# Kernel optimization log

Measured on AMD Instinct MI355X. Metric: run time of the kernel, lower is better.

## Reference

```python
import jax, jax.numpy as jnp
import numpy as np
from jax import lax

ROUTINGS = 3  # num_routing iterations


def _squash(v):
    # v: [..., num_atoms]
    norm = jnp.linalg.norm(v, axis=-1, keepdims=True)
    norm_sq = norm * norm
    return v / norm * (norm_sq / (1.0 + norm_sq))


def setup_inputs() -> dict:
    key = jax.random.key(0)
    k1, k2 = jax.random.split(key)
    B, H, Wd, Ci, Ai = 16, 32, 32, 8, 32
    k, Co, Ao = 5, 16, 16
    x = jax.random.normal(k1, (B, H, Wd, Ci, Ai), dtype=jnp.float32)
    # he_normal init for conv kernel [k, k, Ai, Co*Ao]
    fan_in = k * k * Ai
    W = jax.random.normal(k2, (k, k, Ai, Co * Ao), dtype=jnp.float32) * np.sqrt(2.0 / fan_in).astype(np.float32)
    b = jnp.full((1, 1, Co, Ao), 0.1, dtype=jnp.float32)  # constant(0.1) init
    return {"x": x, "W": W, "b": b}


def reference(x, W, b):
    B, H, Wd, Ci, Ai = x.shape
    k = W.shape[0]
    Co_Ao = W.shape[3]
    Co, Ao = b.shape[2], b.shape[3]
    # fold input capsules into the batch, conv over atoms
    xr = jnp.transpose(x, (0, 3, 1, 2, 4)).reshape(B * Ci, H, Wd, Ai)
    conv = lax.conv_general_dilated(
        xr, W, window_strides=(1, 1), padding="SAME",
        dimension_numbers=("NHWC", "HWIO", "NHWC"))  # [B*Ci, H, W, Co*Ao]
    Ho, Wo = conv.shape[1], conv.shape[2]
    votes = conv.reshape(B, Ci, Ho, Wo, Co, Ao)
    # biases broadcast over spatial dims: [1,1,Co,Ao] -> [Ho,Wo,Co,Ao]
    biases = jnp.broadcast_to(b, (Ho, Wo, Co, Ao))
    # dynamic routing (softmax variant): logits init to 0
    logits = jnp.zeros((B, Ci, Ho, Wo, Co), dtype=votes.dtype)
    activation = None
    for _ in range(ROUTINGS):
        route = jax.nn.softmax(logits, axis=-1)           # [B,Ci,Ho,Wo,Co]
        preact = jnp.sum(route[..., None] * votes, axis=1) + biases  # [B,Ho,Wo,Co,Ao]
        activation = _squash(preact)
        # agreement: sum over atoms of votes * activation
        logits = logits + jnp.sum(votes * activation[:, None], axis=-1)
    return activation
```

## Files before the change

### kernel.cpp

```cpp
#include <hip/hip_runtime.h>
#include <hip/hip_fp16.h>
#include <math.h>


typedef _Float16 f16;
typedef __attribute__((ext_vector_type(2))) _Float16 f16x2;
typedef __attribute__((ext_vector_type(8))) _Float16 f16x8;
typedef __attribute__((ext_vector_type(4))) float f32x4;

#define STRIDE_CI 1944
#define XB_OFF 0
#define WT_OFF 9437184

#define VIDX(p, cp, ao, co) ((((((p)*4 + (cp))*16 + (ao))*18) + (co)) + ((p) & 1))

static __device__ __forceinline__ float2 up16(unsigned int u) {
    union { unsigned int u; f16 h[2]; } c; c.u = u;
    return make_float2((float)c.h[0], (float)c.h[1]);
}

static __device__ __forceinline__ float fdot2u(unsigned int a, unsigned int b, float c) {
#if __has_builtin(__builtin_amdgcn_fdot2)
    union { unsigned int u; f16x2 h; } ua, ub;
    ua.u = a; ub.u = b;
    return __builtin_amdgcn_fdot2(ua.h, ub.h, c, false);
#else
    const float2 fa = up16(a), fb = up16(b);
    return c + fa.x * fb.x + fa.y * fb.y;
#endif
}

__global__ void prep(const float* __restrict__ x, const float* __restrict__ W,
                     f16* __restrict__ xb, f16* __restrict__ Wt) {
    __shared__ f16 lw[32 * 260];
    const int tid = threadIdx.x;
    const int bid = blockIdx.x;
    if (bid < 4608) {
        const int e4 = (bid * 256 + tid) * 4;
        const int c = e4 & 255;
        const int pix = e4 >> 8;
        const int wp = pix % 36;
        const int t = pix / 36;
        const int h = t & 31;
        const int b = t >> 5;
        const int w = wp - 2;
        f16 o[4] = {(f16)0.f, (f16)0.f, (f16)0.f, (f16)0.f};
        if ((unsigned)w < 32u) {
            const float4 v = *(const float4*)&x[(((b * 32 + h) * 32 + w) * 256) + c];
            o[0] = (f16)v.x; o[1] = (f16)v.y; o[2] = (f16)v.z; o[3] = (f16)v.w;
        }
        *(unsigned long long*)&xb[e4] = *(unsigned long long*)o;
    } else {
        const int k5 = bid - 4608;
        for (int rep = 0; rep < 32; ++rep) {
            const int idx = rep * 256 + tid;
            const int ai = idx >> 8, cc = idx & 255;
            lw[ai * 260 + cc] = (f16)W[(k5 * 32 + ai) * 256 + cc];
        }
        __syncthreads();
        for (int rep = 0; rep < 32; ++rep) {
            const int o = rep * 256 + tid;
            const int cc = o >> 5, ai = o & 31;
            Wt[k5 * 8192 + o] = lw[ai * 260 + cc];
        }
    }
}

__global__ __launch_bounds__(256, 3)
void caps_v7(const f16* __restrict__ xb, const f16* __restrict__ Wt,
             const float* __restrict__ bptr, float* __restrict__ out) {
    __shared__ __align__(16) unsigned char smraw[36864];
    f16* patch = (f16*)smraw;
    unsigned int* vl = (unsigned int*)smraw;
    __shared__ __align__(16) uint4 route_l[8 * 16];
    __shared__ float logit_l[8 * 8 * 17];
    __shared__ float bias_l[256];

    const int tid = threadIdx.x;
    const int lane = tid & 63;
    const int wv = tid >> 6;
    const int bid = blockIdx.x;
    const int w0 = (bid & 3) * 8;
    const int h = (bid >> 2) & 31;
    const int b = bid >> 7;

    bias_l[tid] = bptr[tid];

    for (int e = tid; e < 1920; e += 256) {
        const int pos = e >> 5;
        const int ci = (e >> 2) & 7;
        const int s = e & 3;
        const int dh = pos / 12, dw = pos - dh * 12;
        const int gh = h + dh - 2;
        f16x8 v = {};
        if ((unsigned)gh < 32u)
            v = *(const f16x8*)&xb[(((b * 32 + gh) * 36) + (w0 + dw)) * 256 + ci * 32 + s * 8];
        *(f16x8*)&patch[ci * STRIDE_CI + pos * 32 + s * 8] = v;
    }
    __syncthreads();

    const int g = lane >> 4;
    const int q = lane & 15;
    const f16* aptr = patch + (lane & 7) * STRIDE_CI + ((lane >> 3) & 1) * 32 + g * 8;
    const f16* bbase = Wt + (wv * 64 + q) * 32 + g * 8;

    f32x4 acc[4][4];
#pragma unroll
    for (int rb = 0; rb < 4; ++rb)
#pragma unroll
        for (int ct = 0; ct < 4; ++ct) acc[rb][ct] = (f32x4)0.f;

    f16x8 Bc[4], Bn[4];
    f16x8 Ac[4], An[4];
#pragma unroll
    for (int ct = 0; ct < 4; ++ct) {
        Bc[ct] = *(const f16x8*)(bbase + ct * 512);
        Bn[ct] = *(const f16x8*)(bbase + 8192 + ct * 512);
    }
#pragma unroll
    for (int rb = 0; rb < 4; ++rb)
        Ac[rb] = *(const f16x8*)(aptr + rb * 64);

    int k5 = 0;
#pragma unroll
    for (int kh = 0; kh < 5; ++kh) {
#pragma unroll
        for (int kw = 0; kw < 5; ++kw) {
            if (k5 < 24) {
                const int n = k5 + 1;
                const f16* apn = aptr + ((n / 5) * 12 + (n % 5)) * 32;
#pragma unroll
                for (int rb = 0; rb < 4; ++rb)
                    An[rb] = *(const f16x8*)(apn + rb * 64);
            }
            f16x8 Bf[4];
            if (k5 < 23) {
                const f16* bf = bbase + (k5 + 2) * 8192;
#pragma unroll
                for (int ct = 0; ct < 4; ++ct)
                    Bf[ct] = *(const f16x8*)(bf + ct * 512);
            }
#pragma unroll
            for (int rb = 0; rb < 4; ++rb)
#pragma unroll
                for (int ct = 0; ct < 4; ++ct)
                    acc[rb][ct] = __builtin_amdgcn_mfma_f32_16x16x32_f16(
                        Ac[rb], Bc[ct], acc[rb][ct], 0, 0, 0);
#pragma unroll
            for (int rb = 0; rb < 4; ++rb) Ac[rb] = An[rb];
#pragma unroll
            for (int ct = 0; ct < 4; ++ct) { Bc[ct] = Bn[ct]; Bn[ct] = Bf[ct]; }
            ++k5;
        }
    }
    __syncthreads();

#pragma unroll
    for (int rb = 0; rb < 4; ++rb) {
        const int p = rb * 2 + (g >> 1);
        const int cpb = (g & 1) * 2;
#pragma unroll
        for (int ct = 0; ct < 4; ++ct) {
            const int co = wv * 4 + ct;
            union { f16 h[2]; unsigned int u; } c0, c1;
            c0.h[0] = (f16)acc[rb][ct].x; c0.h[1] = (f16)acc[rb][ct].y;
            c1.h[0] = (f16)acc[rb][ct].z; c1.h[1] = (f16)acc[rb][ct].w;
            vl[VIDX(p, cpb, q, co)] = c0.u;
            vl[VIDX(p, cpb + 1, q, co)] = c1.u;
        }
    }
    __syncthreads();

    const int rp  = tid >> 5;
    const int rco = (tid >> 1) & 15;
    const int aoh = tid & 1;
    unsigned int* route_d = (unsigned int*)route_l;

    for (int it = 0; it < 3; ++it) {
        if (it > 0) {
            for (int i = tid; i < 1024; i += 256) {
                const int pp = i >> 7, ci = (i >> 4) & 7, co = i & 15;
                float lg = logit_l[(pp * 8 + ci) * 17 + co];
                float mx = lg;
#pragma unroll
                for (int m = 1; m < 16; m <<= 1) mx = fmaxf(mx, __shfl_xor(mx, m));
                float e = __expf(lg - mx);
                float s = e;
#pragma unroll
                for (int m = 1; m < 16; m <<= 1) s += __shfl_xor(s, m);
                const float r = e * __builtin_amdgcn_rcpf(s);
                const float rother = __shfl_xor(r, 16);
                if (((tid >> 4) & 1) == 0) {
                    union { f16 h[2]; unsigned int u; } pk;
                    pk.h[0] = (f16)r; pk.h[1] = (f16)rother;
                    route_d[(pp * 16 + co) * 4 + (ci >> 1)] = pk.u;
                }
            }
            __syncthreads();
        }

        uint4 r4;
        if (it == 0) {
            r4.x = r4.y = r4.z = r4.w = 0x2C002C00u;
        } else {
            r4 = route_l[rp * 16 + rco];
        }
        float pr[8];
#pragma unroll
        for (int a8 = 0; a8 < 8; ++a8) {
            const int ao = aoh * 8 + a8;
            float v = bias_l[rco * 16 + ao];
            v = fdot2u(vl[VIDX(rp, 0, ao, rco)], r4.x, v);
            v = fdot2u(vl[VIDX(rp, 1, ao, rco)], r4.y, v);
            v = fdot2u(vl[VIDX(rp, 2, ao, rco)], r4.z, v);
            v = fdot2u(vl[VIDX(rp, 3, ao, rco)], r4.w, v);
            pr[a8] = v;
        }
        float sq = 0.f;
#pragma unroll
        for (int a8 = 0; a8 < 8; ++a8) sq += pr[a8] * pr[a8];
        sq += __shfl_xor(sq, 1);
        const float scale = __builtin_amdgcn_sqrtf(sq) * __builtin_amdgcn_rcpf(1.f + sq);
        float actv[8];
#pragma unroll
        for (int a8 = 0; a8 < 8; ++a8) actv[a8] = pr[a8] * scale;

        if (it < 2) {
            float part[8];
#pragma unroll
            for (int cp = 0; cp < 4; ++cp) {
                float e = 0.f, o = 0.f;
#pragma unroll
                for (int a8 = 0; a8 < 8; ++a8) {
                    const float2 f = up16(vl[VIDX(rp, cp, aoh * 8 + a8, rco)]);
                    e += f.x * actv[a8];
                    o += f.y * actv[a8];
                }
                part[cp * 2] = e; part[cp * 2 + 1] = o;
            }
#pragma unroll
            for (int ci = 0; ci < 8; ++ci) part[ci] += __shfl_xor(part[ci], 1);
            if (aoh == 0) {
#pragma unroll
                for (int ci = 0; ci < 8; ++ci) {
                    float* lp = &logit_l[(rp * 8 + ci) * 17 + rco];
                    if (it == 0) *lp = part[ci];
                    else         *lp += part[ci];
                }
            }
            __syncthreads();
        } else {
            const size_t base = ((size_t)((b * 32 + h) * 32 + w0)) * 256;
            float* dst = out + base + rp * 256 + rco * 16 + aoh * 8;
            *(float4*)dst       = make_float4(actv[0], actv[1], actv[2], actv[3]);
            *(float4*)(dst + 4) = make_float4(actv[4], actv[5], actv[6], actv[7]);
        }
    }
}

extern "C" void kernel_launch(void* const* d_in, const int* in_sizes, int n_in,
                              void* d_out, int out_size, void* d_ws, size_t ws_size,
                              hipStream_t stream) {
    const float* x  = (const float*)d_in[0];
    const float* W  = (const float*)d_in[1];
    const float* bb = (const float*)d_in[2];
    float* out = (float*)d_out;
    f16* xb = (f16*)((char*)d_ws + XB_OFF);
    f16* Wt = (f16*)((char*)d_ws + WT_OFF);

    hipLaunchKernelGGL(prep, dim3(4608 + 25), dim3(256), 0, stream, x, W, xb, Wt);
    hipLaunchKernelGGL(caps_v7, dim3(2048), dim3(256), 0, stream, xb, Wt, bb, out);
}
```

Baseline: 147.4 us.

## Keep routing votes in registers via per-thread contiguous LDS layout

Changes the LDS layout of the votes so each routing thread's 32 packed f16 pairs sit contiguously, then loads them once into registers with vector reads instead of re-reading LDS with scattered scalar accesses every routing iteration. Bias values are also loaded straight from global into registers, dropping the shared bias array. This removes repeated LDS traffic in the routing loop but adds about 32 registers per thread, which may pressure the 3-blocks-per-SM launch bound.

```diff
diff --git a/kernel.cpp b/kernel.cpp
--- a/kernel.cpp
+++ b/kernel.cpp
@@ -11,8 +11,6 @@
 #define STRIDE_CI 1944
 #define XB_OFF 0
 #define WT_OFF 9437184
-
-#define VIDX(p, cp, ao, co) ((((((p)*4 + (cp))*16 + (ao))*18) + (co)) + ((p) & 1))
 
 static __device__ __forceinline__ float2 up16(unsigned int u) {
     union { unsigned int u; f16 h[2]; } c; c.u = u;
@@ -67,14 +65,13 @@
 }
 
 __global__ __launch_bounds__(256, 3)
-void caps_v7(const f16* __restrict__ xb, const f16* __restrict__ Wt,
+void caps_v9(const f16* __restrict__ xb, const f16* __restrict__ Wt,
              const float* __restrict__ bptr, float* __restrict__ out) {
     __shared__ __align__(16) unsigned char smraw[36864];
     f16* patch = (f16*)smraw;
     unsigned int* vl = (unsigned int*)smraw;
     __shared__ __align__(16) uint4 route_l[8 * 16];
     __shared__ float logit_l[8 * 8 * 17];
-    __shared__ float bias_l[256];
 
     const int tid = threadIdx.x;
     const int lane = tid & 63;
@@ -84,7 +81,16 @@
     const int h = (bid >> 2) & 31;
     const int b = bid >> 7;
 
-    bias_l[tid] = bptr[tid];
+    const int rp  = tid >> 5;
+    const int rco = (tid >> 1) & 15;
+    const int aoh = tid & 1;
+    float bia[8];
+    {
+        const float4 b0 = *(const float4*)&bptr[rco * 16 + aoh * 8];
+        const float4 b1 = *(const float4*)&bptr[rco * 16 + aoh * 8 + 4];
+        bia[0] = b0.x; bia[1] = b0.y; bia[2] = b0.z; bia[3] = b0.w;
+        bia[4] = b1.x; bia[5] = b1.y; bia[6] = b1.z; bia[7] = b1.w;
+    }
 
     for (int e = tid; e < 1920; e += 256) {
         const int pos = e >> 5;
@@ -159,22 +165,33 @@
     for (int rb = 0; rb < 4; ++rb) {
         const int p = rb * 2 + (g >> 1);
         const int cpb = (g & 1) * 2;
+        const int rowp = p * 32 + (q >> 3);
 #pragma unroll
         for (int ct = 0; ct < 4; ++ct) {
             const int co = wv * 4 + ct;
             union { f16 h[2]; unsigned int u; } c0, c1;
             c0.h[0] = (f16)acc[rb][ct].x; c0.h[1] = (f16)acc[rb][ct].y;
             c1.h[0] = (f16)acc[rb][ct].z; c1.h[1] = (f16)acc[rb][ct].w;
-            vl[VIDX(p, cpb, q, co)] = c0.u;
-            vl[VIDX(p, cpb + 1, q, co)] = c1.u;
+            const int base = (rowp + co * 2) * 36 + cpb * 8 + (q & 7);
+            vl[base] = c0.u;
+            vl[base + 8] = c1.u;
         }
     }
     __syncthreads();
 
-    const int rp  = tid >> 5;
-    const int rco = (tid >> 1) & 15;
-    const int aoh = tid & 1;
+    unsigned int varr[32];
+#pragma unroll
+    for (int cp = 0; cp < 4; ++cp) {
+        const uint4 a = *(const uint4*)&vl[tid * 36 + cp * 8];
+        const uint4 c = *(const uint4*)&vl[tid * 36 + cp * 8 + 4];
+        varr[cp * 8 + 0] = a.x; varr[cp * 8 + 1] = a.y;
+        varr[cp * 8 + 2] = a.z; varr[cp * 8 + 3] = a.w;
+        varr[cp * 8 + 4] = c.x; varr[cp * 8 + 5] = c.y;
+        varr[cp * 8 + 6] = c.z; varr[cp * 8 + 7] = c.w;
+    }
+
     unsigned int* route_d = (unsigned int*)route_l;
+    float actv[8];
 
     for (int it = 0; it < 3; ++it) {
         if (it > 0) {
@@ -208,12 +225,11 @@
         float pr[8];
 #pragma unroll
         for (int a8 = 0; a8 < 8; ++a8) {
-            const int ao = aoh * 8 + a8;
-            float v = bias_l[rco * 16 + ao];
-            v = fdot2u(vl[VIDX(rp, 0, ao, rco)], r4.x, v);
-            v = fdot2u(vl[VIDX(rp, 1, ao, rco)], r4.y, v);
-            v = fdot2u(vl[VIDX(rp, 2, ao, rco)], r4.z, v);
-            v = fdot2u(vl[VIDX(rp, 3, ao, rco)], r4.w, v);
+            float v = bia[a8];
+            v = fdot2u(varr[a8],      r4.x, v);
+            v = fdot2u(varr[8 + a8],  r4.y, v);
+            v = fdot2u(varr[16 + a8], r4.z, v);
+            v = fdot2u(varr[24 + a8], r4.w, v);
             pr[a8] = v;
         }
         float sq = 0.f;
@@ -221,7 +237,6 @@
         for (int a8 = 0; a8 < 8; ++a8) sq += pr[a8] * pr[a8];
         sq += __shfl_xor(sq, 1);
         const float scale = __builtin_amdgcn_sqrtf(sq) * __builtin_amdgcn_rcpf(1.f + sq);
-        float actv[8];
 #pragma unroll
         for (int a8 = 0; a8 < 8; ++a8) actv[a8] = pr[a8] * scale;
 
@@ -232,7 +247,7 @@
                 float e = 0.f, o = 0.f;
 #pragma unroll
                 for (int a8 = 0; a8 < 8; ++a8) {
-                    const float2 f = up16(vl[VIDX(rp, cp, aoh * 8 + a8, rco)]);
+                    const float2 f = up16(varr[cp * 8 + a8]);
                     e += f.x * actv[a8];
                     o += f.y * actv[a8];
                 }
@@ -269,5 +284,5 @@
     f16* Wt = (f16*)((char*)d_ws + WT_OFF);
 
     hipLaunchKernelGGL(prep, dim3(4608 + 25), dim3(256), 0, stream, x, W, xb, Wt);
-    hipLaunchKernelGGL(caps_v7, dim3(2048), dim3(256), 0, stream, xb, Wt, bb, out);
-}
+    hipLaunchKernelGGL(caps_v9, dim3(2048), dim3(256), 0, stream, xb, Wt, bb, out);
+}
```

Result: no change. 145.5 us (-1.3%).
